# Kernel tuning notes

Measured on AMD Instinct MI355X. Metric: run time of the kernel, lower is better.

The kernel has to match this reference:

```python
import jax, jax.numpy as jnp
import numpy as np

CUT0, CUT1 = 20000, 60000
VOCAB = 128000
D = 1024
D1, D2 = 256, 64  # D // 4**i
SZ0, SZ1, SZ2 = CUT0, CUT1 - CUT0, VOCAB - CUT1


def setup_inputs() -> dict:
    key = jax.random.key(0)
    ks = jax.random.split(key, 8)
    ids = jax.random.randint(ks[0], (8, 4096), 0, VOCAB)
    emb0 = jax.random.normal(ks[1], (SZ0, D), dtype=jnp.float32)
    emb1 = jax.random.normal(ks[2], (SZ1, D1), dtype=jnp.float32)
    emb2 = jax.random.normal(ks[3], (SZ2, D2), dtype=jnp.float32)
    # padding_idx=0: row 0 of each cluster table is zero (nn.Embedding semantics)
    emb0 = emb0.at[0].set(0.0)
    emb1 = emb1.at[0].set(0.0)
    emb2 = emb2.at[0].set(0.0)
    # projections, torch Linear: y = x @ W.T + b, init std = dim**-0.5, bias 0
    w1 = jax.random.normal(ks[4], (D, D1), dtype=jnp.float32) * (D1 ** -0.5)
    b1 = jnp.zeros((D,), dtype=jnp.float32)
    w2 = jax.random.normal(ks[5], (D, D2), dtype=jnp.float32) * (D2 ** -0.5)
    b2 = jnp.zeros((D,), dtype=jnp.float32)
    return {"ids": ids, "emb0": emb0, "emb1": emb1, "emb2": emb2,
            "w1": w1, "b1": b1, "w2": w2, "b2": b2}


def reference(ids, emb0, emb1, emb2, w1, b1, w2, b2):
    # cluster masks
    m0 = ids < CUT0
    m2 = ids >= CUT1
    m1 = jnp.logical_and(~m0, ~m2)
    # clamped per-cluster local indices (out-of-cluster rows are masked out below)
    i0 = jnp.clip(ids, 0, SZ0 - 1)
    i1 = jnp.clip(ids - CUT0, 0, SZ1 - 1)
    i2 = jnp.clip(ids - CUT1, 0, SZ2 - 1)
    e0 = emb0[i0]                                   # [B,S,D]
    e1 = jnp.einsum('bsk,dk->bsd', emb1[i1], w1) + b1  # project 256 -> 1024
    e2 = jnp.einsum('bsk,dk->bsd', emb2[i2], w2) + b2  # project  64 -> 1024
    out = (m0[..., None] * e0 + m1[..., None] * e1 + m2[..., None] * e2)
    return out.astype(jnp.float32)
```

## Files before the change

kernel.cpp:

```cpp
#include <hip/hip_runtime.h>

#define CUT0 20000
#define CUT1 60000
#define D    1024
#define D1   256
#define D2   64
#define NTOK 32768

typedef __bf16  bf16x4 __attribute__((ext_vector_type(4)));
typedef __bf16  bf16x8 __attribute__((ext_vector_type(8)));
typedef float   f32x4  __attribute__((ext_vector_type(4)));


__global__ __launch_bounds__(256) void k_classify(
        const int* __restrict__ ids,
        const float* __restrict__ w1,
        const float* __restrict__ w2,
        int* cnt, unsigned* list0, unsigned* list1, unsigned* list2,
        __bf16* __restrict__ w1b, __bf16* __restrict__ w2b) {
    int bid = blockIdx.x, tid = threadIdx.x;
    if (bid < NTOK / 256) {
        unsigned t = bid * 256 + tid;
        int id = ids[t];
        int lane = tid & 63;
        unsigned long long lanebit = 1ull << lane;
        int c = (id < CUT0) ? 0 : (id < CUT1 ? 1 : 2);
        {
            unsigned long long m = __ballot(c == 0);
            if (m) {
                int base = 0;
                if (lane == 0) base = atomicAdd(cnt + 0, __popcll(m));
                base = __shfl(base, 0);
                if (c == 0) list0[base + __popcll(m & (lanebit - 1))] = (t << 17) | (unsigned)id;
            }
        }
        {
            unsigned long long m = __ballot(c == 1);
            if (m) {
                int base = 0;
                if (lane == 0) base = atomicAdd(cnt + 1, __popcll(m));
                base = __shfl(base, 0);
                if (c == 1) list1[base + __popcll(m & (lanebit - 1))] = (t << 17) | (unsigned)(id - CUT0);
            }
        }
        {
            unsigned long long m = __ballot(c == 2);
            if (m) {
                int base = 0;
                if (lane == 0) base = atomicAdd(cnt + 2, __popcll(m));
                base = __shfl(base, 0);
                if (c == 2) list2[base + __popcll(m & (lanebit - 1))] = (t << 17) | (unsigned)(id - CUT1);
            }
        }
    } else {
        int i = (bid - NTOK / 256) * 256 + tid;
        if (i < D1 * D) {
            w1b[i] = (__bf16)w1[i];
        } else {
            int j = i - D1 * D;
            w2b[j] = (__bf16)w2[j];
        }
    }
}

template<int K>
__device__ __forceinline__ void gemm_block(
        const float* __restrict__ emb, const __bf16* __restrict__ wb,
        const float* __restrict__ bias, float* __restrict__ out,
        const unsigned* __restrict__ list, int n, int base, int sd,
        int tid, __bf16* Es, unsigned* plist) {
    constexpr int KS  = K / 32;
    constexpr int SWZ = (K / 8 >= 16) ? 15 : 7;

    if (tid < 64) {
        int li = base + tid;
        plist[tid] = list[li < n ? li : n - 1];
    }
    __syncthreads();

    {
        int r = tid >> 3, q = tid & 7;
        unsigned lidx = plist[r] & 0x1FFFFu;
        const float* src = emb + (size_t)lidx * K + q * (K / 8);
#pragma unroll
        for (int f = 0; f < K / 32; f++) {
            float4 x = *(const float4*)(src + f * 4);
            bf16x4 v = { (__bf16)x.x, (__bf16)x.y, (__bf16)x.z, (__bf16)x.w };
            int k = q * (K / 8) + f * 4;
            int chunk = (k >> 3) ^ (r & SWZ);
            *(bf16x4*)(Es + r * K + chunk * 8 + (k & 7)) = v;
        }
    }
    __syncthreads();

    int lane = tid & 63, wv = tid >> 6;
    int row16 = lane & 15, kg = lane >> 4;
    int wdb = sd + wv * 64;

    f32x4 acc[4][4];
#pragma unroll
    for (int t = 0; t < 4; t++)
#pragma unroll
        for (int c = 0; c < 4; c++) acc[t][c] = (f32x4){0.f, 0.f, 0.f, 0.f};

#pragma unroll
    for (int ks = 0; ks < KS; ks++) {
        bf16x8 b[4];
#pragma unroll
        for (int c = 0; c < 4; c++) {
            int r = c * 16 + row16;
            int chunk = (kg + ks * 4) ^ (r & SWZ);
            b[c] = *(const bf16x8*)(Es + r * K + chunk * 8);
        }
#pragma unroll
        for (int t = 0; t < 4; t++) {
            bf16x8 a = *(const bf16x8*)(wb + (size_t)(wdb + t * 16 + row16) * K + kg * 8 + ks * 32);
#pragma unroll
            for (int c = 0; c < 4; c++)
                acc[t][c] = __builtin_amdgcn_mfma_f32_16x16x32_bf16(a, b[c], acc[t][c], 0, 0, 0);
        }
    }

#pragma unroll
    for (int t = 0; t < 4; t++) {
        int d0 = wdb + t * 16 + kg * 4;
        float4 bs = *(const float4*)(bias + d0);
#pragma unroll
        for (int c = 0; c < 4; c++) {
            int ti = c * 16 + row16;
            if (base + ti < n) {
                unsigned p = plist[ti];
                float4 o = { acc[t][c][0] + bs.x, acc[t][c][1] + bs.y,
                             acc[t][c][2] + bs.z, acc[t][c][3] + bs.w };
                *(float4*)(out + (size_t)(p >> 17) * D + d0) = o;
            }
        }
    }
}

__global__ __launch_bounds__(512, 4) void k_fused(
        const float* __restrict__ emb0,
        const float* __restrict__ emb1,
        const float* __restrict__ emb2,
        const float* __restrict__ b1,
        const float* __restrict__ b2,
        float* __restrict__ out,
        const int* __restrict__ cnt,
        const unsigned* __restrict__ list0,
        const unsigned* __restrict__ list1,
        const unsigned* __restrict__ list2,
        const __bf16* __restrict__ w1b,
        const __bf16* __restrict__ w2b) {
    __shared__ __bf16 Es[64 * 256];
    __shared__ unsigned plist[64];

    int bid = blockIdx.x, tid = threadIdx.x;
    if (bid < 1024) {
        int n = cnt[1];
        int base = (bid >> 1) * 64;
        if (base >= n) return;
        gemm_block<D1>(emb1, w1b, b1, out, list1, n, base, (bid & 1) * 512, tid, Es, plist);
    } else if (bid < 2048) {
        int n = cnt[2];
        int b = bid - 1024;
        int base = (b >> 1) * 64;
        if (base >= n) return;
        gemm_block<D2>(emb2, w2b, b2, out, list2, n, base, (b & 1) * 512, tid, Es, plist);
    } else {
        int n0 = cnt[0];
        int f = tid & 255;
        for (int r = (bid - 2048) * 2 + (tid >> 8); r < n0; r += 512) {
            unsigned p = list0[r];
            const float4* src = (const float4*)(emb0 + (size_t)(p & 0x1FFFFu) * D);
            float4* dst = (float4*)(out + (size_t)(p >> 17) * D);
            dst[f] = src[f];
        }
    }
}

extern "C" void kernel_launch(void* const* d_in, const int* in_sizes, int n_in,
                              void* d_out, int out_size, void* d_ws, size_t ws_size,
                              hipStream_t stream) {
    const int*   ids  = (const int*)d_in[0];
    const float* emb0 = (const float*)d_in[1];
    const float* emb1 = (const float*)d_in[2];
    const float* emb2 = (const float*)d_in[3];
    const float* w1   = (const float*)d_in[4];
    const float* b1   = (const float*)d_in[5];
    const float* w2   = (const float*)d_in[6];
    const float* b2   = (const float*)d_in[7];
    float* out = (float*)d_out;

    int* cnt        = (int*)d_ws;
    unsigned* list0 = (unsigned*)((char*)d_ws + 256);
    unsigned* list1 = list0 + NTOK;
    unsigned* list2 = list1 + NTOK;
    __bf16* w1b     = (__bf16*)(list2 + NTOK);
    __bf16* w2b     = w1b + (size_t)D * D1;

    hipMemsetAsync(cnt, 0, 3 * sizeof(int), stream);
    hipLaunchKernelGGL(k_classify, dim3(NTOK / 256 + 1280), dim3(256), 0, stream,
                       ids, w1, w2, cnt, list0, list1, list2, w1b, w2b);
    hipLaunchKernelGGL(k_fused, dim3(2304), dim3(512), 0, stream,
                       emb0, emb1, emb2, b1, b2, out, cnt,
                       list0, list1, list2, w1b, w2b);
}
```

Before: 73.69 us.

## Stage weight slices in LDS and stream token embeddings directly into MFMA

Reorganizes the projection GEMMs so each block keeps a 64-row slice of the bf16 weight matrix resident in shared memory. Warps then loop over groups of 16 tokens, loading the embedding rows straight from global memory into MFMA B operands. Before, each block staged 64 tokens' embeddings in LDS and read weights from global memory, so weights were re-fetched for every token tile. The grid shrinks from 2304 to 896 persistent-style blocks. The cost is that each embedding row is now read by 16 blocks (one per output slice), and each wave handles only 16 tokens per pass.

```diff
diff --git a/kernel.cpp b/kernel.cpp
--- a/kernel.cpp
+++ b/kernel.cpp
@@ -7,7 +7,6 @@
 #define D2   64
 #define NTOK 32768
 
-typedef __bf16  bf16x4 __attribute__((ext_vector_type(4)));
 typedef __bf16  bf16x8 __attribute__((ext_vector_type(8)));
 typedef float   f32x4  __attribute__((ext_vector_type(4)));
 
@@ -64,81 +63,66 @@
 }
 
 template<int K>
-__device__ __forceinline__ void gemm_block(
-        const float* __restrict__ emb, const __bf16* __restrict__ wb,
-        const float* __restrict__ bias, float* __restrict__ out,
-        const unsigned* __restrict__ list, int n, int base, int sd,
-        int tid, __bf16* Es, unsigned* plist) {
+__device__ __forceinline__ void stream_gemm(
+        const float* __restrict__ emb, const float* __restrict__ bias,
+        float* __restrict__ out, const unsigned* __restrict__ list, int n,
+        const __bf16* __restrict__ wb, int s, int bi, int nstride,
+        int tid, __bf16* Ws) {
     constexpr int KS  = K / 32;
-    constexpr int SWZ = (K / 8 >= 16) ? 15 : 7;
+    constexpr int CH  = K / 8;
+    constexpr int SWZ = (CH >= 16) ? 15 : 7;
 
-    if (tid < 64) {
-        int li = base + tid;
-        plist[tid] = list[li < n ? li : n - 1];
-    }
-    __syncthreads();
-
-    {
-        int r = tid >> 3, q = tid & 7;
-        unsigned lidx = plist[r] & 0x1FFFFu;
-        const float* src = emb + (size_t)lidx * K + q * (K / 8);
-#pragma unroll
-        for (int f = 0; f < K / 32; f++) {
-            float4 x = *(const float4*)(src + f * 4);
-            bf16x4 v = { (__bf16)x.x, (__bf16)x.y, (__bf16)x.z, (__bf16)x.w };
-            int k = q * (K / 8) + f * 4;
-            int chunk = (k >> 3) ^ (r & SWZ);
-            *(bf16x4*)(Es + r * K + chunk * 8 + (k & 7)) = v;
-        }
+    for (int idx = tid; idx < 64 * CH; idx += 512) {
+        int r = idx / CH, c = idx % CH;
+        bf16x8 v = *(const bf16x8*)(wb + (size_t)(s * 64 + r) * K + c * 8);
+        *(bf16x8*)(Ws + r * K + ((c ^ (r & SWZ)) * 8)) = v;
     }
     __syncthreads();
 
     int lane = tid & 63, wv = tid >> 6;
-    int row16 = lane & 15, kg = lane >> 4;
-    int wdb = sd + wv * 64;
+    int col = lane & 15, kg = lane >> 4;
+    int ng = (n + 15) >> 4;
 
-    f32x4 acc[4][4];
+    for (int g = bi * 8 + wv; g < ng; g += nstride) {
+        int ti = g * 16 + col;
+        unsigned p = list[ti < n ? ti : n - 1];
+        unsigned lidx = p & 0x1FFFFu, tok = p >> 17;
+        const float* ep = emb + (size_t)lidx * K + kg * 8;
+
+        f32x4 acc[4];
 #pragma unroll
-    for (int t = 0; t < 4; t++)
-#pragma unroll
-        for (int c = 0; c < 4; c++) acc[t][c] = (f32x4){0.f, 0.f, 0.f, 0.f};
+        for (int t = 0; t < 4; t++) acc[t] = (f32x4){0.f, 0.f, 0.f, 0.f};
 
 #pragma unroll
-    for (int ks = 0; ks < KS; ks++) {
-        bf16x8 b[4];
+        for (int ks = 0; ks < KS; ks++) {
+            float4 x = *(const float4*)(ep + ks * 32);
+            float4 y = *(const float4*)(ep + ks * 32 + 4);
+            bf16x8 b;
+            b[0] = (__bf16)x.x; b[1] = (__bf16)x.y; b[2] = (__bf16)x.z; b[3] = (__bf16)x.w;
+            b[4] = (__bf16)y.x; b[5] = (__bf16)y.y; b[6] = (__bf16)y.z; b[7] = (__bf16)y.w;
 #pragma unroll
-        for (int c = 0; c < 4; c++) {
-            int r = c * 16 + row16;
-            int chunk = (kg + ks * 4) ^ (r & SWZ);
-            b[c] = *(const bf16x8*)(Es + r * K + chunk * 8);
+            for (int t = 0; t < 4; t++) {
+                int dl = t * 16 + col;
+                int ch = (kg + ks * 4) ^ (dl & SWZ);
+                bf16x8 a = *(const bf16x8*)(Ws + dl * K + ch * 8);
+                acc[t] = __builtin_amdgcn_mfma_f32_16x16x32_bf16(a, b, acc[t], 0, 0, 0);
+            }
         }
+
+        if (ti < n) {
+            float* orow = out + (size_t)tok * D + s * 64 + kg * 4;
 #pragma unroll
-        for (int t = 0; t < 4; t++) {
-            bf16x8 a = *(const bf16x8*)(wb + (size_t)(wdb + t * 16 + row16) * K + kg * 8 + ks * 32);
-#pragma unroll
-            for (int c = 0; c < 4; c++)
-                acc[t][c] = __builtin_amdgcn_mfma_f32_16x16x32_bf16(a, b[c], acc[t][c], 0, 0, 0);
-        }
-    }
-
-#pragma unroll
-    for (int t = 0; t < 4; t++) {
-        int d0 = wdb + t * 16 + kg * 4;
-        float4 bs = *(const float4*)(bias + d0);
-#pragma unroll
-        for (int c = 0; c < 4; c++) {
-            int ti = c * 16 + row16;
-            if (base + ti < n) {
-                unsigned p = plist[ti];
-                float4 o = { acc[t][c][0] + bs.x, acc[t][c][1] + bs.y,
-                             acc[t][c][2] + bs.z, acc[t][c][3] + bs.w };
-                *(float4*)(out + (size_t)(p >> 17) * D + d0) = o;
+            for (int t = 0; t < 4; t++) {
+                float4 bs = *(const float4*)(bias + s * 64 + t * 16 + kg * 4);
+                float4 o = { acc[t][0] + bs.x, acc[t][1] + bs.y,
+                             acc[t][2] + bs.z, acc[t][3] + bs.w };
+                *(float4*)(orow + t * 16) = o;
             }
         }
     }
 }
 
-__global__ __launch_bounds__(512, 4) void k_fused(
+__global__ __launch_bounds__(512, 4) void k_stream(
         const float* __restrict__ emb0,
         const float* __restrict__ emb1,
         const float* __restrict__ emb2,
@@ -151,30 +135,27 @@
         const unsigned* __restrict__ list2,
         const __bf16* __restrict__ w1b,
         const __bf16* __restrict__ w2b) {
-    __shared__ __bf16 Es[64 * 256];
-    __shared__ unsigned plist[64];
+    __shared__ __bf16 Ws[64 * 256];
 
     int bid = blockIdx.x, tid = threadIdx.x;
-    if (bid < 1024) {
-        int n = cnt[1];
-        int base = (bid >> 1) * 64;
-        if (base >= n) return;
-        gemm_block<D1>(emb1, w1b, b1, out, list1, n, base, (bid & 1) * 512, tid, Es, plist);
-    } else if (bid < 2048) {
-        int n = cnt[2];
-        int b = bid - 1024;
-        int base = (b >> 1) * 64;
-        if (base >= n) return;
-        gemm_block<D2>(emb2, w2b, b2, out, list2, n, base, (b & 1) * 512, tid, Es, plist);
-    } else {
+
+    if (bid < 256) {
         int n0 = cnt[0];
         int f = tid & 255;
-        for (int r = (bid - 2048) * 2 + (tid >> 8); r < n0; r += 512) {
+        for (int r = bid * 2 + (tid >> 8); r < n0; r += 512) {
             unsigned p = list0[r];
             const float4* src = (const float4*)(emb0 + (size_t)(p & 0x1FFFFu) * D);
             float4* dst = (float4*)(out + (size_t)(p >> 17) * D);
             dst[f] = src[f];
         }
+    } else if (bid < 512) {
+        int e = bid - 256;
+        stream_gemm<D1>(emb1, b1, out, list1, cnt[1], w1b,
+                        e & 15, e >> 4, 16 * 8, tid, Ws);
+    } else {
+        int e = bid - 512;
+        stream_gemm<D2>(emb2, b2, out, list2, cnt[2], w2b,
+                        e & 15, e >> 4, 24 * 8, tid, Ws);
     }
 }
 
@@ -201,7 +182,7 @@
     hipMemsetAsync(cnt, 0, 3 * sizeof(int), stream);
     hipLaunchKernelGGL(k_classify, dim3(NTOK / 256 + 1280), dim3(256), 0, stream,
                        ids, w1, w2, cnt, list0, list1, list2, w1b, w2b);
-    hipLaunchKernelGGL(k_fused, dim3(2304), dim3(512), 0, stream,
+    hipLaunchKernelGGL(k_stream, dim3(896), dim3(512), 0, stream,
                        emb0, emb1, emb2, b1, b2, out, cnt,
                        list0, list1, list2, w1b, w2b);
 }
```

Result: slower. 104.8 us (+42.1%).

## Double-buffer gathered embeddings across 1024-thread blocks computing full output width

Applied to the files above, without the earlier changes.

Each GEMM block now has 16 waves covering all 1024 output columns and processes two 64-token tiles. The second tile's embedding gather is held in registers while the first tile's MFMA work runs, then written to a second LDS buffer. The emb0 copy path prefetches the next list entry, and the grid shrinks from 2304 blocks of 512 threads to 768 blocks of 1024. This aims to hide gather latency and reduce launch and block count, at the cost of doubled LDS, more registers per thread and lower occupancy per CU.

```diff
diff --git a/kernel.cpp b/kernel.cpp
--- a/kernel.cpp
+++ b/kernel.cpp
@@ -64,38 +64,43 @@
 }
 
 template<int K>
-__device__ __forceinline__ void gemm_block(
-        const float* __restrict__ emb, const __bf16* __restrict__ wb,
-        const float* __restrict__ bias, float* __restrict__ out,
-        const unsigned* __restrict__ list, int n, int base, int sd,
-        int tid, __bf16* Es, unsigned* plist) {
+__device__ __forceinline__ void stage_regs(
+        const float* __restrict__ emb, const unsigned* __restrict__ list,
+        int n, int base, int tid, float4* v, unsigned* pout) {
+    int r = tid >> 4, q = tid & 15;
+    int li = base + r; if (li >= n) li = n - 1;
+    unsigned p = list[li];
+    *pout = p;
+    const float* src = emb + (size_t)(p & 0x1FFFFu) * K + q * (K / 16);
+#pragma unroll
+    for (int f = 0; f < K / 64; f++) v[f] = ((const float4*)src)[f];
+}
+
+template<int K>
+__device__ __forceinline__ void write_lds(
+        __bf16* __restrict__ Ebuf, unsigned* __restrict__ plistbuf,
+        int tid, const float4* v, unsigned p) {
+    constexpr int SWZ = (K / 8 >= 16) ? 15 : 7;
+    int r = tid >> 4, q = tid & 15;
+    if (q == 0) plistbuf[r] = p;
+#pragma unroll
+    for (int f = 0; f < K / 64; f++) {
+        bf16x4 w = { (__bf16)v[f].x, (__bf16)v[f].y, (__bf16)v[f].z, (__bf16)v[f].w };
+        int k = q * (K / 16) + f * 4;
+        int chunk = (k >> 3) ^ (r & SWZ);
+        *(bf16x4*)(Ebuf + r * K + chunk * 8 + (k & 7)) = w;
+    }
+}
+
+template<int K>
+__device__ __forceinline__ void mfma_store(
+        const __bf16* __restrict__ Ebuf, const unsigned* __restrict__ plistbuf,
+        const __bf16* __restrict__ wb, const float* __restrict__ bias,
+        float* __restrict__ out, int n, int base, int lane, int wv) {
     constexpr int KS  = K / 32;
     constexpr int SWZ = (K / 8 >= 16) ? 15 : 7;
-
-    if (tid < 64) {
-        int li = base + tid;
-        plist[tid] = list[li < n ? li : n - 1];
-    }
-    __syncthreads();
-
-    {
-        int r = tid >> 3, q = tid & 7;
-        unsigned lidx = plist[r] & 0x1FFFFu;
-        const float* src = emb + (size_t)lidx * K + q * (K / 8);
-#pragma unroll
-        for (int f = 0; f < K / 32; f++) {
-            float4 x = *(const float4*)(src + f * 4);
-            bf16x4 v = { (__bf16)x.x, (__bf16)x.y, (__bf16)x.z, (__bf16)x.w };
-            int k = q * (K / 8) + f * 4;
-            int chunk = (k >> 3) ^ (r & SWZ);
-            *(bf16x4*)(Es + r * K + chunk * 8 + (k & 7)) = v;
-        }
-    }
-    __syncthreads();
-
-    int lane = tid & 63, wv = tid >> 6;
     int row16 = lane & 15, kg = lane >> 4;
-    int wdb = sd + wv * 64;
+    int wdb = wv * 64;
 
     f32x4 acc[4][4];
 #pragma unroll
@@ -108,9 +113,9 @@
         bf16x8 b[4];
 #pragma unroll
         for (int c = 0; c < 4; c++) {
-            int r = c * 16 + row16;
-            int chunk = (kg + ks * 4) ^ (r & SWZ);
-            b[c] = *(const bf16x8*)(Es + r * K + chunk * 8);
+            int rr = c * 16 + row16;
+            int ch = (kg + ks * 4) ^ (rr & SWZ);
+            b[c] = *(const bf16x8*)(Ebuf + rr * K + ch * 8);
         }
 #pragma unroll
         for (int t = 0; t < 4; t++) {
@@ -122,23 +127,53 @@
     }
 
 #pragma unroll
-    for (int t = 0; t < 4; t++) {
-        int d0 = wdb + t * 16 + kg * 4;
-        float4 bs = *(const float4*)(bias + d0);
-#pragma unroll
-        for (int c = 0; c < 4; c++) {
-            int ti = c * 16 + row16;
-            if (base + ti < n) {
-                unsigned p = plist[ti];
+    for (int c = 0; c < 4; c++) {
+        int ti = c * 16 + row16;
+        if (base + ti < n) {
+            unsigned p = plistbuf[ti];
+            float* orow = out + (size_t)(p >> 17) * D;
+#pragma unroll
+            for (int t = 0; t < 4; t++) {
+                int d0 = wdb + t * 16 + kg * 4;
+                float4 bs = *(const float4*)(bias + d0);
                 float4 o = { acc[t][c][0] + bs.x, acc[t][c][1] + bs.y,
                              acc[t][c][2] + bs.z, acc[t][c][3] + bs.w };
-                *(float4*)(out + (size_t)(p >> 17) * D + d0) = o;
-            }
-        }
-    }
-}
-
-__global__ __launch_bounds__(512, 4) void k_fused(
+                *(float4*)(orow + d0) = o;
+            }
+        }
+    }
+}
+
+template<int K>
+__device__ __forceinline__ void gemm_role(
+        const float* __restrict__ emb, const __bf16* __restrict__ wb,
+        const float* __restrict__ bias, const unsigned* __restrict__ list,
+        int n, int b, float* __restrict__ out, int tid,
+        __bf16 (*Es)[64 * 256], unsigned (*plist)[64]) {
+    int baseA = b * 128;
+    if (baseA >= n) return;
+    int baseB = baseA + 64;
+    int lane = tid & 63, wv = tid >> 6;
+
+    float4 vA[4]; unsigned pA;
+    stage_regs<K>(emb, list, n, baseA, tid, vA, &pA);
+    write_lds<K>(Es[0], plist[0], tid, vA, pA);
+    __syncthreads();
+
+    bool hasB = baseB < n;
+    float4 vB[4]; unsigned pB = 0;
+    if (hasB) stage_regs<K>(emb, list, n, baseB, tid, vB, &pB);
+
+    mfma_store<K>(Es[0], plist[0], wb, bias, out, n, baseA, lane, wv);
+
+    if (hasB) {
+        write_lds<K>(Es[1], plist[1], tid, vB, pB);
+        __syncthreads();
+        mfma_store<K>(Es[1], plist[1], wb, bias, out, n, baseB, lane, wv);
+    }
+}
+
+__global__ __launch_bounds__(1024) void k_work(
         const float* __restrict__ emb0,
         const float* __restrict__ emb1,
         const float* __restrict__ emb2,
@@ -151,31 +186,33 @@
         const unsigned* __restrict__ list2,
         const __bf16* __restrict__ w1b,
         const __bf16* __restrict__ w2b) {
-    __shared__ __bf16 Es[64 * 256];
-    __shared__ unsigned plist[64];
+    __shared__ __bf16 Es[2][64 * 256];
+    __shared__ unsigned plist[2][64];
 
     int bid = blockIdx.x, tid = threadIdx.x;
-    if (bid < 1024) {
-        int n = cnt[1];
-        int base = (bid >> 1) * 64;
-        if (base >= n) return;
-        gemm_block<D1>(emb1, w1b, b1, out, list1, n, base, (bid & 1) * 512, tid, Es, plist);
-    } else if (bid < 2048) {
-        int n = cnt[2];
-        int b = bid - 1024;
-        int base = (b >> 1) * 64;
-        if (base >= n) return;
-        gemm_block<D2>(emb2, w2b, b2, out, list2, n, base, (b & 1) * 512, tid, Es, plist);
-    } else {
+
+    if (bid < 256) {
         int n0 = cnt[0];
         int f = tid & 255;
-        for (int r = (bid - 2048) * 2 + (tid >> 8); r < n0; r += 512) {
-            unsigned p = list0[r];
+        int r = bid * 4 + (tid >> 8);
+        if (r >= n0) return;
+        unsigned p = list0[r];
+        for (;;) {
+            int rn = r + 1024;
+            unsigned pn = (rn < n0) ? list0[rn] : 0u;
             const float4* src = (const float4*)(emb0 + (size_t)(p & 0x1FFFFu) * D);
             float4* dst = (float4*)(out + (size_t)(p >> 17) * D);
             dst[f] = src[f];
-        }
-    }
+            if (rn >= n0) break;
+            r = rn; p = pn;
+        }
+        return;
+    }
+
+    if (bid < 512)
+        gemm_role<D1>(emb1, w1b, b1, list1, cnt[1], bid - 256, out, tid, Es, plist);
+    else
+        gemm_role<D2>(emb2, w2b, b2, list2, cnt[2], bid - 512, out, tid, Es, plist);
 }
 
 extern "C" void kernel_launch(void* const* d_in, const int* in_sizes, int n_in,
@@ -201,7 +238,7 @@
     hipMemsetAsync(cnt, 0, 3 * sizeof(int), stream);
     hipLaunchKernelGGL(k_classify, dim3(NTOK / 256 + 1280), dim3(256), 0, stream,
                        ids, w1, w2, cnt, list0, list1, list2, w1b, w2b);
-    hipLaunchKernelGGL(k_fused, dim3(2304), dim3(512), 0, stream,
+    hipLaunchKernelGGL(k_work, dim3(768), dim3(1024), 0, stream,
                        emb0, emb1, emb2, b1, b2, out, cnt,
                        list0, list1, list2, w1b, w2b);
 }
```

Result: slower. 115.3 us (+56.4%).

## Stage GEMM outputs through LDS for row-contiguous stores; schedule copy blocks first

Applied to the files above, without the earlier changes.

The GEMM epilogue now writes each wave's accumulator tiles, with bias added, into a swizzled LDS slab and reads them back transposed. Each 16-lane group can then store a contiguous 256-byte segment of an output row, instead of scattered float4 writes. Block order is also changed so the emb0 gather/copy blocks are dispatched before the GEMM blocks, which may balance the tail better. The cost is an extra barrier and an LDS round trip per tile.

```diff
diff --git a/kernel.cpp b/kernel.cpp
--- a/kernel.cpp
+++ b/kernel.cpp
@@ -84,7 +84,7 @@
         const float* src = emb + (size_t)lidx * K + q * (K / 8);
 #pragma unroll
         for (int f = 0; f < K / 32; f++) {
-            float4 x = *(const float4*)(src + f * 4);
+            float4 x = ((const float4*)src)[f];
             bf16x4 v = { (__bf16)x.x, (__bf16)x.y, (__bf16)x.z, (__bf16)x.w };
             int k = q * (K / 8) + f * 4;
             int chunk = (k >> 3) ^ (r & SWZ);
@@ -108,9 +108,9 @@
         bf16x8 b[4];
 #pragma unroll
         for (int c = 0; c < 4; c++) {
-            int r = c * 16 + row16;
-            int chunk = (kg + ks * 4) ^ (r & SWZ);
-            b[c] = *(const bf16x8*)(Es + r * K + chunk * 8);
+            int rr = c * 16 + row16;
+            int ch = (kg + ks * 4) ^ (rr & SWZ);
+            b[c] = *(const bf16x8*)(Es + rr * K + ch * 8);
         }
 #pragma unroll
         for (int t = 0; t < 4; t++) {
@@ -121,24 +121,36 @@
         }
     }
 
-#pragma unroll
-    for (int t = 0; t < 4; t++) {
-        int d0 = wdb + t * 16 + kg * 4;
-        float4 bs = *(const float4*)(bias + d0);
-#pragma unroll
-        for (int c = 0; c < 4; c++) {
-            int ti = c * 16 + row16;
-            if (base + ti < n) {
-                unsigned p = plist[ti];
-                float4 o = { acc[t][c][0] + bs.x, acc[t][c][1] + bs.y,
-                             acc[t][c][2] + bs.z, acc[t][c][3] + bs.w };
-                *(float4*)(out + (size_t)(p >> 17) * D + d0) = o;
-            }
-        }
-    }
-}
-
-__global__ __launch_bounds__(512, 4) void k_fused(
+    __syncthreads();
+
+    float* slab = (float*)Es + wv * 1024;
+#pragma unroll
+    for (int c = 0; c < 4; c++) {
+#pragma unroll
+        for (int t = 0; t < 4; t++) {
+            float4 bs = *(const float4*)(bias + wdb + t * 16 + kg * 4);
+            f32x4 v = acc[t][c];
+            v[0] += bs.x; v[1] += bs.y; v[2] += bs.z; v[3] += bs.w;
+            int phys = (((t ^ (row16 >> 2)) & 3) << 2) | ((kg ^ row16) & 3);
+            *(f32x4*)(slab + row16 * 64 + phys * 4) = v;
+        }
+#pragma unroll
+        for (int i = 0; i < 4; i++) {
+            int tk = i * 4 + (lane >> 4);
+            int lc = lane & 15;
+            int phys = ((((lc >> 2) ^ (tk >> 2)) & 3) << 2) | ((lc ^ tk) & 3);
+            f32x4 v = *(const f32x4*)(slab + tk * 64 + phys * 4);
+            int lt = c * 16 + tk;
+            if (base + lt < n) {
+                unsigned p = plist[lt];
+                float4 o = { v[0], v[1], v[2], v[3] };
+                *(float4*)(out + (size_t)(p >> 17) * D + wdb + lc * 4) = o;
+            }
+        }
+    }
+}
+
+__global__ __launch_bounds__(512, 4) void k_work(
         const float* __restrict__ emb0,
         const float* __restrict__ emb1,
         const float* __restrict__ emb2,
@@ -155,26 +167,31 @@
     __shared__ unsigned plist[64];
 
     int bid = blockIdx.x, tid = threadIdx.x;
-    if (bid < 1024) {
-        int n = cnt[1];
-        int base = (bid >> 1) * 64;
-        if (base >= n) return;
-        gemm_block<D1>(emb1, w1b, b1, out, list1, n, base, (bid & 1) * 512, tid, Es, plist);
-    } else if (bid < 2048) {
-        int n = cnt[2];
-        int b = bid - 1024;
-        int base = (b >> 1) * 64;
-        if (base >= n) return;
-        gemm_block<D2>(emb2, w2b, b2, out, list2, n, base, (b & 1) * 512, tid, Es, plist);
-    } else {
+
+    if (bid < 256) {
         int n0 = cnt[0];
         int f = tid & 255;
-        for (int r = (bid - 2048) * 2 + (tid >> 8); r < n0; r += 512) {
+        for (int r = bid * 2 + (tid >> 8); r < n0; r += 512) {
             unsigned p = list0[r];
             const float4* src = (const float4*)(emb0 + (size_t)(p & 0x1FFFFu) * D);
             float4* dst = (float4*)(out + (size_t)(p >> 17) * D);
             dst[f] = src[f];
         }
+        return;
+    }
+
+    if (bid < 1280) {
+        int e = bid - 256;
+        int n = cnt[1];
+        int base = (e >> 1) * 64;
+        if (base >= n) return;
+        gemm_block<D1>(emb1, w1b, b1, out, list1, n, base, (e & 1) * 512, tid, Es, plist);
+    } else {
+        int e = bid - 1280;
+        int n = cnt[2];
+        int base = (e >> 1) * 64;
+        if (base >= n) return;
+        gemm_block<D2>(emb2, w2b, b2, out, list2, n, base, (e & 1) * 512, tid, Es, plist);
     }
 }
 
@@ -201,7 +218,7 @@
     hipMemsetAsync(cnt, 0, 3 * sizeof(int), stream);
     hipLaunchKernelGGL(k_classify, dim3(NTOK / 256 + 1280), dim3(256), 0, stream,
                        ids, w1, w2, cnt, list0, list1, list2, w1b, w2b);
-    hipLaunchKernelGGL(k_fused, dim3(2304), dim3(512), 0, stream,
+    hipLaunchKernelGGL(k_work, dim3(2304), dim3(512), 0, stream,
                        emb0, emb1, emb2, b1, b2, out, cnt,
                        list0, list1, list2, w1b, w2b);
 }
```

Measured after the change: 64.45 us. 12.5% less time.
